# Kernel optimization log

Measured on AMD Instinct MI355X. Metric: run time of the kernel, lower is better.

Reference implementation:

```python
import jax, jax.numpy as jnp
import numpy as np

DROPOUT_P = 0.5  # pre-softmax dropout prob from __init__
_MASK_KEY = jax.random.key(42)  # fixed key -> deterministic dropout mask


def setup_inputs() -> dict:
    key = jax.random.key(0)
    kq, kk, kv = jax.random.split(key, 3)
    shape = (4, 16, 1024, 64)  # [B, H, S, D]
    Q = jax.random.normal(kq, shape, dtype=jnp.float32)
    K = jax.random.normal(kk, shape, dtype=jnp.float32)
    V = jax.random.normal(kv, shape, dtype=jnp.float32)
    return {"Q": Q, "K": K, "V": V}


def reference(Q, K, V):
    # scores: [B, H, S, S] = Q @ K^T  (no 1/sqrt(d) scaling: scale=False)
    scores = jnp.einsum("bhqd,bhkd->bhqk", Q, K)
    # pre-softmax dropout (train mode, p=0.5), deterministic fixed-key mask
    keep = jax.random.bernoulli(_MASK_KEY, 1.0 - DROPOUT_P, scores.shape)
    scores = jnp.where(keep, scores / (1.0 - DROPOUT_P), 0.0)
    attn = jax.nn.softmax(scores, axis=-1)
    return jnp.einsum("bhqk,bhkd->bhqd", attn, V)
```

## Files before the change

### kernel.cpp

```cpp
#include <hip/hip_runtime.h>
#include <hip/hip_bf16.h>
#include <hip/hip_fp16.h>
#include <math.h>

typedef _Float16 f16x8 __attribute__((ext_vector_type(8)));
typedef __fp16  h16x2 __attribute__((ext_vector_type(2)));
typedef float f32x4 __attribute__((ext_vector_type(4)));

#define S_LEN 1024
#define DH 64
#define KVB 64
#define NIT 16
#define KROW 72
#define THR 11.0f

__device__ __forceinline__ unsigned rotl(unsigned x, unsigned r) {
  return __builtin_amdgcn_alignbit(x, x, 32u - r);
}

__device__ __forceinline__ bool keep_bit(unsigned e) {
  const unsigned ks1 = 42u;
  const unsigned ks2 = 0x1BD11BF0u;
  unsigned x0 = 0u;
  unsigned x1 = e + ks1;
#define TFR(Ra,Rb,Rc,Rd) \
  x0 += x1; x1 = rotl(x1, Ra); x1 ^= x0; \
  x0 += x1; x1 = rotl(x1, Rb); x1 ^= x0; \
  x0 += x1; x1 = rotl(x1, Rc); x1 ^= x0; \
  x0 += x1; x1 = rotl(x1, Rd); x1 ^= x0;
  TFR(13u,15u,26u, 6u)  x0 += ks1; x1 += ks2 + 1u;
  TFR(17u,29u,16u,24u)  x0 += ks2; x1 += 2u;
  TFR(13u,15u,26u, 6u)     x1 += ks1 + 3u;
  TFR(17u,29u,16u,24u)  x0 += ks1; x1 += ks2 + 4u;
  TFR(13u,15u,26u, 6u)  x0 += ks2; x1 += 5u;
#undef TFR
  return ((x0 ^ x1) >> 31) == 0u;
}

__device__ __forceinline__ f16x8 pk8(f32x4 a, f32x4 b) {
  h16x2 p0 = __builtin_amdgcn_cvt_pkrtz(a[0], a[1]);
  h16x2 p1 = __builtin_amdgcn_cvt_pkrtz(a[2], a[3]);
  h16x2 p2 = __builtin_amdgcn_cvt_pkrtz(b[0], b[1]);
  h16x2 p3 = __builtin_amdgcn_cvt_pkrtz(b[2], b[3]);
  f16x8 r;
  r[0]=(_Float16)p0[0]; r[1]=(_Float16)p0[1]; r[2]=(_Float16)p1[0]; r[3]=(_Float16)p1[1];
  r[4]=(_Float16)p2[0]; r[5]=(_Float16)p2[1]; r[6]=(_Float16)p3[0]; r[7]=(_Float16)p3[1];
  return r;
}

__global__ __launch_bounds__(256)
void attn_dropout_kernel(const float* __restrict__ Q, const float* __restrict__ K,
                         const float* __restrict__ V, float* __restrict__ out) {
  __shared__ _Float16 Kl[KVB][KROW];
  __shared__ _Float16 Vt[DH][KROW];
  __shared__ _Float16 Pl[4][16][KROW];

  const unsigned bh   = blockIdx.x >> 4;
  const unsigned q0   = (blockIdx.x & 15u) * 64u;
  const unsigned tid  = threadIdx.x;
  const unsigned w    = tid >> 6;
  const unsigned lane = tid & 63u;
  const unsigned g    = lane >> 4;
  const unsigned ln   = lane & 15u;
  const unsigned qw   = q0 + w * 16u;

  f16x8 Qa0, Qa1;
  {
    const float* Qp = Q + (size_t)(bh * S_LEN + qw + ln) * DH + g * 8;
    const float s = 2.885390082f;
    f32x4 a = *(const f32x4*)(Qp)      * s;
    f32x4 b = *(const f32x4*)(Qp + 4)  * s;
    f32x4 c = *(const f32x4*)(Qp + 32) * s;
    f32x4 d = *(const f32x4*)(Qp + 36) * s;
    Qa0 = pk8(a, b);
    Qa1 = pk8(c, d);
  }

  float mrun[4], lpart[4];
  f32x4 accO[4];
#pragma unroll
  for (int r = 0; r < 4; ++r) { mrun[r] = -1e30f; lpart[r] = 0.0f; }
#pragma unroll
  for (int n = 0; n < 4; ++n) accO[n] = (f32x4){0.f, 0.f, 0.f, 0.f};

  const unsigned kk  = tid >> 2;
  const unsigned dgf = (tid & 3u) * 16u;

  f32x4 kr0, kr1, kr2, kr3, vr0, vr1, vr2, vr3;
  {
    const float* Kp = K + (size_t)(bh * S_LEN + kk) * DH + dgf;
    kr0 = *(const f32x4*)(Kp);  kr1 = *(const f32x4*)(Kp + 4);
    kr2 = *(const f32x4*)(Kp + 8); kr3 = *(const f32x4*)(Kp + 12);
    const float* Vp = V + (size_t)(bh * S_LEN + kk) * DH + dgf;
    vr0 = *(const f32x4*)(Vp);  vr1 = *(const f32x4*)(Vp + 4);
    vr2 = *(const f32x4*)(Vp + 8); vr3 = *(const f32x4*)(Vp + 12);
  }

  for (int t = 0; t < NIT; ++t) {
    __syncthreads();
    *(f16x8*)&Kl[kk][dgf]     = pk8(kr0, kr1);
    *(f16x8*)&Kl[kk][dgf + 8] = pk8(kr2, kr3);
#pragma unroll
    for (int i = 0; i < 4; ++i) {
      Vt[dgf +  0 + i][kk] = (_Float16)vr0[i];
      Vt[dgf +  4 + i][kk] = (_Float16)vr1[i];
      Vt[dgf +  8 + i][kk] = (_Float16)vr2[i];
      Vt[dgf + 12 + i][kk] = (_Float16)vr3[i];
    }
    __syncthreads();

    {
      int tn = (t + 1 < NIT) ? t + 1 : NIT - 1;
      const float* Kp = K + (size_t)(bh * S_LEN + tn * KVB + kk) * DH + dgf;
      kr0 = *(const f32x4*)(Kp);  kr1 = *(const f32x4*)(Kp + 4);
      kr2 = *(const f32x4*)(Kp + 8); kr3 = *(const f32x4*)(Kp + 12);
      const float* Vp = V + (size_t)(bh * S_LEN + tn * KVB + kk) * DH + dgf;
      vr0 = *(const f32x4*)(Vp);  vr1 = *(const f32x4*)(Vp + 4);
      vr2 = *(const f32x4*)(Vp + 8); vr3 = *(const f32x4*)(Vp + 12);
    }

    f32x4 sc[4];
#pragma unroll
    for (int nt = 0; nt < 4; ++nt) {
      f16x8 kb0 = *(const f16x8*)&Kl[nt * 16 + ln][g * 8];
      f16x8 kb1 = *(const f16x8*)&Kl[nt * 16 + ln][32 + g * 8];
      f32x4 a = (f32x4){0.f, 0.f, 0.f, 0.f};
      a = __builtin_amdgcn_mfma_f32_16x16x32_f16(Qa0, kb0, a, 0, 0, 0);
      a = __builtin_amdgcn_mfma_f32_16x16x32_f16(Qa1, kb1, a, 0, 0, 0);
      sc[nt] = a;
    }

    float sm[4][4];
    float pmx[4];
#pragma unroll
    for (int r = 0; r < 4; ++r) pmx[r] = -1e30f;
#pragma unroll
    for (int nt = 0; nt < 4; ++nt) {
#pragma unroll
      for (int r = 0; r < 4; ++r) {
        unsigned q  = qw + g * 4 + r;
        unsigned kg = (unsigned)t * KVB + nt * 16 + ln;
        unsigned e  = (bh << 20) + (q << 10) + kg;
        float v = keep_bit(e) ? sc[nt][r] : 0.0f;
        sm[nt][r] = v;
        pmx[r] = fmaxf(pmx[r], v);
      }
    }

    bool need = (pmx[0] > mrun[0] + THR) | (pmx[1] > mrun[1] + THR) |
                (pmx[2] > mrun[2] + THR) | (pmx[3] > mrun[3] + THR);
    if (__any(need)) {
#pragma unroll
      for (int r = 0; r < 4; ++r) {
        float mx = pmx[r];
#pragma unroll
        for (int off = 1; off < 16; off <<= 1) mx = fmaxf(mx, __shfl_xor(mx, off));
        float mn  = fmaxf(mrun[r], mx);
        float scl = exp2f(mrun[r] - mn);
        mrun[r] = mn;
        lpart[r] *= scl;
#pragma unroll
        for (int n = 0; n < 4; ++n) accO[n][r] *= scl;
      }
    }

    float ps[4][4];
#pragma unroll
    for (int nt = 0; nt < 4; ++nt) {
#pragma unroll
      for (int r = 0; r < 4; ++r) {
        float p = exp2f(sm[nt][r] - mrun[r]);
        ps[nt][r] = p;
        lpart[r] += p;
      }
    }

#pragma unroll
    for (int nt = 0; nt < 4; ++nt)
#pragma unroll
      for (int r = 0; r < 4; ++r)
        Pl[w][g * 4 + r][nt * 16 + ln] = (_Float16)ps[nt][r];

    f16x8 Pa0 = *(const f16x8*)&Pl[w][ln][g * 8];
    f16x8 Pa1 = *(const f16x8*)&Pl[w][ln][32 + g * 8];
#pragma unroll
    for (int nd = 0; nd < 4; ++nd) {
      f16x8 vb0 = *(const f16x8*)&Vt[nd * 16 + ln][g * 8];
      f16x8 vb1 = *(const f16x8*)&Vt[nd * 16 + ln][32 + g * 8];
      accO[nd] = __builtin_amdgcn_mfma_f32_16x16x32_f16(Pa0, vb0, accO[nd], 0, 0, 0);
      accO[nd] = __builtin_amdgcn_mfma_f32_16x16x32_f16(Pa1, vb1, accO[nd], 0, 0, 0);
    }
  }

  float lf[4];
#pragma unroll
  for (int r = 0; r < 4; ++r) {
    float l = lpart[r];
#pragma unroll
    for (int off = 1; off < 16; off <<= 1) l += __shfl_xor(l, off);
    lf[r] = l;
  }
#pragma unroll
  for (int nd = 0; nd < 4; ++nd) {
#pragma unroll
    for (int r = 0; r < 4; ++r) {
      unsigned q = qw + g * 4 + r;
      out[(size_t)(bh * S_LEN + q) * DH + nd * 16 + ln] = accO[nd][r] / lf[r];
    }
  }
}

extern "C" void kernel_launch(void* const* d_in, const int* in_sizes, int n_in,
                              void* d_out, int out_size, void* d_ws, size_t ws_size,
                              hipStream_t stream) {
  const float* Q = (const float*)d_in[0];
  const float* K = (const float*)d_in[1];
  const float* V = (const float*)d_in[2];
  float* out = (float*)d_out;
  dim3 grid(64 * 16);
  dim3 block(256);
  hipLaunchKernelGGL(attn_dropout_kernel, grid, block, 0, stream, Q, K, V, out);
}
```

Measured before the change: 242.2 us.

## Load V operands directly from global memory instead of staging through LDS

Removes the transposed V tile in shared memory and its scalar transpose stores. Each wave now gathers the V MFMA B-operand straight from global memory with strided scalar loads, converting to fp16 in registers. This cuts LDS traffic and LDS usage. In exchange, every wave loads V separately with uncoalesced 4-byte loads (stride of DH floats), issued in the same iteration they are used instead of being prefetched.

```diff
diff --git a/kernel.cpp b/kernel.cpp
--- a/kernel.cpp
+++ b/kernel.cpp
@@ -52,7 +52,6 @@
 void attn_dropout_kernel(const float* __restrict__ Q, const float* __restrict__ K,
                          const float* __restrict__ V, float* __restrict__ out) {
   __shared__ _Float16 Kl[KVB][KROW];
-  __shared__ _Float16 Vt[DH][KROW];
   __shared__ _Float16 Pl[4][16][KROW];
 
   const unsigned bh   = blockIdx.x >> 4;
@@ -86,27 +85,19 @@
   const unsigned kk  = tid >> 2;
   const unsigned dgf = (tid & 3u) * 16u;
 
-  f32x4 kr0, kr1, kr2, kr3, vr0, vr1, vr2, vr3;
+  f32x4 kr0, kr1, kr2, kr3;
   {
     const float* Kp = K + (size_t)(bh * S_LEN + kk) * DH + dgf;
     kr0 = *(const f32x4*)(Kp);  kr1 = *(const f32x4*)(Kp + 4);
     kr2 = *(const f32x4*)(Kp + 8); kr3 = *(const f32x4*)(Kp + 12);
-    const float* Vp = V + (size_t)(bh * S_LEN + kk) * DH + dgf;
-    vr0 = *(const f32x4*)(Vp);  vr1 = *(const f32x4*)(Vp + 4);
-    vr2 = *(const f32x4*)(Vp + 8); vr3 = *(const f32x4*)(Vp + 12);
-  }
+  }
+
+  const float* Vg_base = V + (size_t)bh * S_LEN * DH + g * 8 * DH + ln;
 
   for (int t = 0; t < NIT; ++t) {
     __syncthreads();
     *(f16x8*)&Kl[kk][dgf]     = pk8(kr0, kr1);
     *(f16x8*)&Kl[kk][dgf + 8] = pk8(kr2, kr3);
-#pragma unroll
-    for (int i = 0; i < 4; ++i) {
-      Vt[dgf +  0 + i][kk] = (_Float16)vr0[i];
-      Vt[dgf +  4 + i][kk] = (_Float16)vr1[i];
-      Vt[dgf +  8 + i][kk] = (_Float16)vr2[i];
-      Vt[dgf + 12 + i][kk] = (_Float16)vr3[i];
-    }
     __syncthreads();
 
     {
@@ -114,9 +105,24 @@
       const float* Kp = K + (size_t)(bh * S_LEN + tn * KVB + kk) * DH + dgf;
       kr0 = *(const f32x4*)(Kp);  kr1 = *(const f32x4*)(Kp + 4);
       kr2 = *(const f32x4*)(Kp + 8); kr3 = *(const f32x4*)(Kp + 12);
-      const float* Vp = V + (size_t)(bh * S_LEN + tn * KVB + kk) * DH + dgf;
-      vr0 = *(const f32x4*)(Vp);  vr1 = *(const f32x4*)(Vp + 4);
-      vr2 = *(const f32x4*)(Vp + 8); vr3 = *(const f32x4*)(Vp + 12);
+    }
+
+    f16x8 vb0[4], vb1[4];
+    {
+      const float* Vg = Vg_base + (size_t)t * KVB * DH;
+#pragma unroll
+      for (int nd = 0; nd < 4; ++nd) {
+        f32x4 a, b, c, d;
+#pragma unroll
+        for (int j = 0; j < 4; ++j) {
+          a[j] = Vg[(j)      * DH + nd * 16];
+          b[j] = Vg[(4 + j)  * DH + nd * 16];
+          c[j] = Vg[(32 + j) * DH + nd * 16];
+          d[j] = Vg[(36 + j) * DH + nd * 16];
+        }
+        vb0[nd] = pk8(a, b);
+        vb1[nd] = pk8(c, d);
+      }
     }
 
     f32x4 sc[4];
@@ -185,10 +191,8 @@
     f16x8 Pa1 = *(const f16x8*)&Pl[w][ln][32 + g * 8];
 #pragma unroll
     for (int nd = 0; nd < 4; ++nd) {
-      f16x8 vb0 = *(const f16x8*)&Vt[nd * 16 + ln][g * 8];
-      f16x8 vb1 = *(const f16x8*)&Vt[nd * 16 + ln][32 + g * 8];
-      accO[nd] = __builtin_amdgcn_mfma_f32_16x16x32_f16(Pa0, vb0, accO[nd], 0, 0, 0);
-      accO[nd] = __builtin_amdgcn_mfma_f32_16x16x32_f16(Pa1, vb1, accO[nd], 0, 0, 0);
+      accO[nd] = __builtin_amdgcn_mfma_f32_16x16x32_f16(Pa0, vb0[nd], accO[nd], 0, 0, 0);
+      accO[nd] = __builtin_amdgcn_mfma_f32_16x16x32_f16(Pa1, vb1[nd], accO[nd], 0, 0, 0);
     }
   }
 
```

Result: slower. 251.3 us (+3.8%).

## Split KV sequence in two halves with partial outputs and merge kernel

Applied to the files above, without the earlier changes.

Splits each attention block's key/value range into two halves processed by separate blocks, doubling the grid to 2048 blocks. Each block writes unnormalized partial outputs plus running max and sum to workspace, and a second merge kernel combines them with rescaling. This raises parallelism and occupancy on a GPU with many CUs, at the cost of extra workspace traffic (about 2x output size) and a second launch. It falls back to the original single-pass kernel when the workspace is too small.

```diff
diff --git a/kernel.cpp b/kernel.cpp
--- a/kernel.cpp
+++ b/kernel.cpp
@@ -10,9 +10,15 @@
 #define S_LEN 1024
 #define DH 64
 #define KVB 64
-#define NIT 16
 #define KROW 72
 #define THR 11.0f
+
+#define NBH 64
+#define NQT 16
+#define NBLK (NBH*NQT)
+#define OPART_FLOATS ((size_t)2 * NBLK * 64 * 64)
+#define ML_FLOATS    ((size_t)2 * NBLK * 64 * 2)
+#define WS_NEED ((OPART_FLOATS + ML_FLOATS) * 4)
 
 __device__ __forceinline__ unsigned rotl(unsigned x, unsigned r) {
   return __builtin_amdgcn_alignbit(x, x, 32u - r);
@@ -48,15 +54,16 @@
   return r;
 }
 
-__global__ __launch_bounds__(256)
-void attn_dropout_kernel(const float* __restrict__ Q, const float* __restrict__ K,
-                         const float* __restrict__ V, float* __restrict__ out) {
+template <bool PARTIAL>
+__device__ __forceinline__ void attn_core(
+    const float* __restrict__ Q, const float* __restrict__ K,
+    const float* __restrict__ V, float* __restrict__ out,
+    float* __restrict__ Opart, float* __restrict__ ML,
+    unsigned bh, unsigned q0, unsigned pbase, int t0, int nt_cnt) {
   __shared__ _Float16 Kl[KVB][KROW];
   __shared__ _Float16 Vt[DH][KROW];
   __shared__ _Float16 Pl[4][16][KROW];
 
-  const unsigned bh   = blockIdx.x >> 4;
-  const unsigned q0   = (blockIdx.x & 15u) * 64u;
   const unsigned tid  = threadIdx.x;
   const unsigned w    = tid >> 6;
   const unsigned lane = tid & 63u;
@@ -88,15 +95,15 @@
 
   f32x4 kr0, kr1, kr2, kr3, vr0, vr1, vr2, vr3;
   {
-    const float* Kp = K + (size_t)(bh * S_LEN + kk) * DH + dgf;
+    const float* Kp = K + (size_t)(bh * S_LEN + t0 * KVB + kk) * DH + dgf;
     kr0 = *(const f32x4*)(Kp);  kr1 = *(const f32x4*)(Kp + 4);
     kr2 = *(const f32x4*)(Kp + 8); kr3 = *(const f32x4*)(Kp + 12);
-    const float* Vp = V + (size_t)(bh * S_LEN + kk) * DH + dgf;
+    const float* Vp = V + (size_t)(bh * S_LEN + t0 * KVB + kk) * DH + dgf;
     vr0 = *(const f32x4*)(Vp);  vr1 = *(const f32x4*)(Vp + 4);
     vr2 = *(const f32x4*)(Vp + 8); vr3 = *(const f32x4*)(Vp + 12);
   }
 
-  for (int t = 0; t < NIT; ++t) {
+  for (int t = t0; t < t0 + nt_cnt; ++t) {
     __syncthreads();
     *(f16x8*)&Kl[kk][dgf]     = pk8(kr0, kr1);
     *(f16x8*)&Kl[kk][dgf + 8] = pk8(kr2, kr3);
@@ -110,7 +117,7 @@
     __syncthreads();
 
     {
-      int tn = (t + 1 < NIT) ? t + 1 : NIT - 1;
+      int tn = (t + 1 < t0 + nt_cnt) ? t + 1 : t;
       const float* Kp = K + (size_t)(bh * S_LEN + tn * KVB + kk) * DH + dgf;
       kr0 = *(const f32x4*)(Kp);  kr1 = *(const f32x4*)(Kp + 4);
       kr2 = *(const f32x4*)(Kp + 8); kr3 = *(const f32x4*)(Kp + 12);
@@ -200,13 +207,80 @@
     for (int off = 1; off < 16; off <<= 1) l += __shfl_xor(l, off);
     lf[r] = l;
   }
-#pragma unroll
-  for (int nd = 0; nd < 4; ++nd) {
-#pragma unroll
-    for (int r = 0; r < 4; ++r) {
-      unsigned q = qw + g * 4 + r;
-      out[(size_t)(bh * S_LEN + q) * DH + nd * 16 + ln] = accO[nd][r] / lf[r];
-    }
+
+  if (PARTIAL) {
+#pragma unroll
+    for (int nd = 0; nd < 4; ++nd)
+#pragma unroll
+      for (int r = 0; r < 4; ++r) {
+        unsigned row = w * 16u + g * 4u + r;
+        Opart[((size_t)pbase * 64 + row) * 64 + nd * 16 + ln] = accO[nd][r];
+      }
+    if (ln == 0) {
+#pragma unroll
+      for (int r = 0; r < 4; ++r) {
+        unsigned row = w * 16u + g * 4u + r;
+        ML[((size_t)pbase * 64 + row) * 2 + 0] = mrun[r];
+        ML[((size_t)pbase * 64 + row) * 2 + 1] = lf[r];
+      }
+    }
+  } else {
+#pragma unroll
+    for (int nd = 0; nd < 4; ++nd)
+#pragma unroll
+      for (int r = 0; r < 4; ++r) {
+        unsigned q = qw + g * 4 + r;
+        out[(size_t)(bh * S_LEN + q) * DH + nd * 16 + ln] = accO[nd][r] / lf[r];
+      }
+  }
+}
+
+__global__ __launch_bounds__(256)
+void attn_partial_kernel(const float* __restrict__ Q, const float* __restrict__ K,
+                         const float* __restrict__ V, float* __restrict__ Opart,
+                         float* __restrict__ ML) {
+  const unsigned bid  = blockIdx.x;
+  const unsigned half = bid >> 10;
+  const unsigned bh   = (bid & 1023u) >> 4;
+  const unsigned q0   = (bid & 15u) * 64u;
+  attn_core<true>(Q, K, V, nullptr, Opart, ML, bh, q0, bid, half * 8, 8);
+}
+
+__global__ __launch_bounds__(256)
+void attn_full_kernel(const float* __restrict__ Q, const float* __restrict__ K,
+                      const float* __restrict__ V, float* __restrict__ out) {
+  const unsigned bh = blockIdx.x >> 4;
+  const unsigned q0 = (blockIdx.x & 15u) * 64u;
+  attn_core<false>(Q, K, V, out, nullptr, nullptr, bh, q0, 0, 0, 16);
+}
+
+__global__ __launch_bounds__(256)
+void attn_merge_kernel(const float* __restrict__ Opart, const float* __restrict__ ML,
+                       float* __restrict__ out) {
+  const unsigned tid   = threadIdx.x;
+  const unsigned row_g = blockIdx.x * 64u + (tid >> 2);
+  const unsigned cg    = (tid & 3u) * 16u;
+  const unsigned bh = row_g >> 10;
+  const unsigned q  = row_g & 1023u;
+  const unsigned qt = q >> 6;
+  const unsigned ql = q & 63u;
+  const unsigned b0 = bh * 16u + qt;
+  const unsigned b1 = 1024u + b0;
+  float m0 = ML[((size_t)b0 * 64 + ql) * 2 + 0];
+  float l0 = ML[((size_t)b0 * 64 + ql) * 2 + 1];
+  float m1 = ML[((size_t)b1 * 64 + ql) * 2 + 0];
+  float l1 = ML[((size_t)b1 * 64 + ql) * 2 + 1];
+  float m  = fmaxf(m0, m1);
+  float s0 = exp2f(m0 - m), s1 = exp2f(m1 - m);
+  float inv = 1.0f / (l0 * s0 + l1 * s1);
+  const float* P0 = Opart + ((size_t)b0 * 64 + ql) * 64 + cg;
+  const float* P1 = Opart + ((size_t)b1 * 64 + ql) * 64 + cg;
+  float* Po = out + (size_t)row_g * 64 + cg;
+#pragma unroll
+  for (int j = 0; j < 4; ++j) {
+    f32x4 a = *(const f32x4*)(P0 + j * 4);
+    f32x4 b = *(const f32x4*)(P1 + j * 4);
+    *(f32x4*)(Po + j * 4) = (a * s0 + b * s1) * inv;
   }
 }
 
@@ -217,7 +291,15 @@
   const float* K = (const float*)d_in[1];
   const float* V = (const float*)d_in[2];
   float* out = (float*)d_out;
-  dim3 grid(64 * 16);
-  dim3 block(256);
-  hipLaunchKernelGGL(attn_dropout_kernel, grid, block, 0, stream, Q, K, V, out);
-}
+  if (ws_size >= WS_NEED) {
+    float* Opart = (float*)d_ws;
+    float* ML    = Opart + OPART_FLOATS;
+    hipLaunchKernelGGL(attn_partial_kernel, dim3(2 * NBLK), dim3(256), 0, stream,
+                       Q, K, V, Opart, ML);
+    hipLaunchKernelGGL(attn_merge_kernel, dim3(1024), dim3(256), 0, stream,
+                       Opart, ML, out);
+  } else {
+    hipLaunchKernelGGL(attn_full_kernel, dim3(NBLK), dim3(256), 0, stream,
+                       Q, K, V, out);
+  }
+}
```

After: 250.5 us. 3.4% more time.
